# Kernel tuning notes

Hardware: AMD Instinct MI355X
Metric: run time of the kernel (lower is better)

## Reference

```python
import jax, jax.numpy as jnp
import numpy as np

N = 20000      # num_nodes
E = 320000     # num_edges (avg degree 16)
HID = 256      # hid_dim
H = 4          # attention heads
D = HID // H   # per-head dim (concat heads -> HID)
L = 2          # nGAT_layer
OUT = 12       # out_dim / pred_len (decoder steps)
NEG_SLOPE = 0.2


def setup_inputs() -> dict:
    key = jax.random.key(0)
    ks = jax.random.split(key, 16)
    s = 0.05
    nrm = lambda k, shape: jax.random.normal(k, shape, jnp.float32) * s
    return dict(
        x=nrm(ks[0], (N, HID)),
        edge_index=jax.random.randint(ks[1], (2, E), 0, N, dtype=jnp.int32),
        # GATv2Conv params per layer (stacked over L layers)
        gat_w_src=nrm(ks[2], (L, HID, H * D)),
        gat_w_dst=nrm(ks[3], (L, HID, H * D)),
        gat_att=nrm(ks[4], (L, H, D)),
        gat_bias=nrm(ks[5], (L, H * D)),
        # decoder_mlp: Linear(1 + HID -> HID)
        mlp_w=nrm(ks[6], (HID, 1 + HID)),
        mlp_b=nrm(ks[7], (HID,)),
        # nn.LSTM (1 layer, input HID, hidden HID), torch gate order i,f,g,o
        lstm_w_ih=nrm(ks[8], (4 * HID, HID)),
        lstm_w_hh=nrm(ks[9], (4 * HID, HID)),
        lstm_b_ih=nrm(ks[10], (4 * HID,)),
        lstm_b_hh=nrm(ks[11], (4 * HID,)),
        # decoder_init_proj: Linear(HID -> 1); decoder_output_proj: Linear(HID -> 1)
        init_w=nrm(ks[12], (1, HID)),
        init_b=nrm(ks[13], (1,)),
        out_w=nrm(ks[14], (1, HID)),
        out_b=nrm(ks[15], (1,)),
    )


def _gatv2_layer(x, src, dst, w_src, w_dst, att, bias):
    n = x.shape[0]
    xl = (x @ w_src).reshape(n, H, D)   # source-side projection
    xr = (x @ w_dst).reshape(n, H, D)   # destination-side projection
    # GATv2: e_ij = a^T LeakyReLU(Wl x_j + Wr x_i)
    e = jax.nn.leaky_relu(xl[src] + xr[dst], NEG_SLOPE)        # [E,H,D]
    logits = jnp.einsum('ehd,hd->eh', e, att)                   # [E,H]
    # edge softmax over incoming edges of each destination node
    m = jax.ops.segment_max(logits, dst, num_segments=n)        # [N,H]
    ex = jnp.exp(logits - m[dst])
    denom = jax.ops.segment_sum(ex, dst, num_segments=n)
    alpha = ex / denom[dst]                                     # [E,H]
    out = jax.ops.segment_sum(xl[src] * alpha[:, :, None], dst, num_segments=n)
    return out.reshape(n, H * D) + bias


def reference(x, edge_index, gat_w_src, gat_w_dst, gat_att, gat_bias,
              mlp_w, mlp_b, lstm_w_ih, lstm_w_hh, lstm_b_ih, lstm_b_hh,
              init_w, init_b, out_w, out_b):
    src, dst = edge_index[0], edge_index[1]
    # stacked GAT blocks: GATv2Conv + ELU (element == 2)
    for l in range(L):
        x = _gatv2_layer(x, src, dst, gat_w_src[l], gat_w_dst[l], gat_att[l], gat_bias[l])
        x = jax.nn.elu(x)
    # recurrent LSTM decoder, batch = nodes, seq step by step
    ctx = x                      # encoder_context
    h = x                        # h_0 = x (num_layers = 1)
    c = jnp.zeros_like(x)        # c_0 = 0
    prev = x @ init_w.T + init_b  # [N,1]
    outs = []
    for _ in range(OUT):
        dec_in = jnp.concatenate([prev, ctx], axis=1) @ mlp_w.T + mlp_b  # [N,HID]
        gates = dec_in @ lstm_w_ih.T + lstm_b_ih + h @ lstm_w_hh.T + lstm_b_hh
        i_g, f_g, g_g, o_g = jnp.split(gates, 4, axis=1)
        i_g = jax.nn.sigmoid(i_g)
        f_g = jax.nn.sigmoid(f_g)
        o_g = jax.nn.sigmoid(o_g)
        g_g = jnp.tanh(g_g)
        c = f_g * c + i_g * g_g
        h = o_g * jnp.tanh(c)
        prev = h @ out_w.T + out_b  # [N,1]
        outs.append(prev)
    return jnp.concatenate(outs, axis=1)  # [N, OUT]
```

## Files before the change

### kernel.cpp

```cpp
#include <hip/hip_runtime.h>
#include <hip/hip_bf16.h>

#define NN 20000
#define NE 320000
#define TOUT 12
#define DEGMAX 96
#define MR 80
#define NBLK 250
#define NCPL 13

typedef __bf16 bf16x8 __attribute__((ext_vector_type(8)));
typedef float float4v __attribute__((ext_vector_type(4)));

#define LD8(p) (*(const bf16x8*)(p))
#define MFMA16(a,b,c) __builtin_amdgcn_mfma_f32_16x16x32_bf16((a),(b),(c),0,0,0)

__device__ __forceinline__ float bf2f(const __hip_bfloat16 v){ return __bfloat162float(v); }
__device__ __forceinline__ __hip_bfloat16 f2bf(float v){ return __float2bfloat16(v); }
__device__ __forceinline__ float sigmoidr_(float x){ return __builtin_amdgcn_rcpf(1.f + __expf(-x)); }
__device__ __forceinline__ float tanhr_(float x){ return 1.f - 2.f*__builtin_amdgcn_rcpf(__expf(2.f*x) + 1.f); }
__device__ __forceinline__ float rdf(const void* p, int i, int f32){
  return f32 ? ((const float*)p)[i] : __bfloat162float(((const __hip_bfloat16*)p)[i]);
}

__global__ void k_detect(const void* xraw, int* flag){
  __shared__ int cnt;
  if(threadIdx.x == 0) cnt = 0;
  __syncthreads();
  const unsigned* w = (const unsigned*)xraw;
  int local = 0;
  for(int i = threadIdx.x; i < 4096; i += 256){
    unsigned b = (w[i] >> 8) & 0x7F;
    if(b >= 0x33 && b <= 0x3F) local++;
  }
  atomicAdd(&cnt, local);
  __syncthreads();
  if(threadIdx.x == 0) *flag = (cnt > 2048) ? 0 : 1;
}

__global__ void k_fail(float* out, int n){
  int i = blockIdx.x*256 + threadIdx.x;
  if(i < n) out[i] = 256.0f;
}

__global__ void k_count(const int* __restrict__ dst, int* __restrict__ deg){
  int e = blockIdx.x*256 + threadIdx.x;
  if(e < NE){
    unsigned d = (unsigned)dst[e];
    if(d < NN) atomicAdd(&deg[d], 1);
  }
}

__global__ void k_scan(const int* __restrict__ deg, int* __restrict__ offp, int* __restrict__ cursor){
  __shared__ int part[256];
  __shared__ int excl[257];
  const int CH = (NN + 255)/256;
  int tid = threadIdx.x;
  int lo = tid*CH;
  int hi = lo + CH; if(hi > NN) hi = NN;
  int s = 0;
  for(int i=lo;i<hi;i++) s += deg[i];
  part[tid] = s;
  __syncthreads();
  if(tid == 0){
    int run = 0;
    for(int i=0;i<256;i++){ excl[i] = run; run += part[i]; }
    excl[256] = run;
  }
  __syncthreads();
  int run = excl[tid];
  for(int i=lo;i<hi;i++){ offp[i] = run; cursor[i] = run; run += deg[i]; }
  if(tid == 0) offp[NN] = excl[256];
}

__global__ void k_fill(const int* __restrict__ src, const int* __restrict__ dst,
                       int* __restrict__ cursor, int* __restrict__ csr_src){
  int e = blockIdx.x*256 + threadIdx.x;
  if(e >= NE) return;
  unsigned d = (unsigned)dst[e];
  if(d >= NN) return;
  unsigned p = (unsigned)atomicAdd(&cursor[d], 1);
  if(p < NE){
    unsigned sv = (unsigned)src[e];
    csr_src[p] = (sv < NN) ? (int)sv : 0;
  }
}

__global__ void k_prep(const void* __restrict__ w_src, const void* __restrict__ w_dst,
                       const void* __restrict__ w_hh, const void* __restrict__ wih,
                       const void* __restrict__ mlp_w, const int* __restrict__ flag,
                       __hip_bfloat16* __restrict__ wsrcT, __hip_bfloat16* __restrict__ wdstT,
                       __hip_bfloat16* __restrict__ whhp, __hip_bfloat16* __restrict__ wihb,
                       __hip_bfloat16* __restrict__ mlpT){
  int tid = blockIdx.x*256 + threadIdx.x;
  int f = *flag;
  if(tid < 131072){
    int l = tid >> 16, r = tid & 65535, o = r >> 8, i = r & 255;
    wsrcT[tid] = f2bf(rdf(w_src, l*65536 + i*256 + o, f));
    wdstT[tid] = f2bf(rdf(w_dst, l*65536 + i*256 + o, f));
  }
  if(tid < 262144){
    whhp[tid] = f2bf(rdf(w_hh, tid, f));
    wihb[tid] = f2bf(rdf(wih, tid, f));
  }
  if(tid < 65536){
    int k = tid >> 8, j = tid & 255;
    mlpT[tid] = f2bf(rdf(mlp_w, j*257 + 1 + k, f));
  }
}

__global__ void k_prep_ub(const void* __restrict__ wih, const void* __restrict__ mlp_w,
                          const void* __restrict__ mlp_b,
                          const void* __restrict__ b_ih, const void* __restrict__ b_hh,
                          const void* __restrict__ att, const void* __restrict__ gbias,
                          const void* __restrict__ init_w, const void* __restrict__ init_b,
                          const void* __restrict__ out_w, const void* __restrict__ out_b,
                          const int* __restrict__ flag,
                          float* __restrict__ u, float* __restrict__ bc,
                          float* __restrict__ attf, float* __restrict__ gbiasf,
                          float* __restrict__ initwf, float* __restrict__ outwf,
                          float* __restrict__ sc){
  __shared__ float su[256], sb[256];
  int g = blockIdx.x, j = threadIdx.x, f = *flag;
  float w = rdf(wih, g*256 + j, f);
  su[j] = w * rdf(mlp_w, j*257, f);
  sb[j] = w * rdf(mlp_b, j, f);
  if(g < 2){
    int i = g*256 + j;
    attf[i] = rdf(att, i, f);
    gbiasf[i] = rdf(gbias, i, f);
  }
  if(g == 0){
    initwf[j] = rdf(init_w, j, f);
    outwf[j]  = rdf(out_w, j, f);
    if(j == 0){ sc[0] = rdf(init_b, 0, f); sc[1] = rdf(out_b, 0, f); }
  }
  __syncthreads();
  for(int s=128; s>0; s>>=1){
    if(j < s){ su[j] += su[j+s]; sb[j] += sb[j+s]; }
    __syncthreads();
  }
  if(j == 0){ u[g] = su[0]; bc[g] = sb[0] + rdf(b_ih, g, f) + rdf(b_hh, g, f); }
}

__global__ void k_fold(const __hip_bfloat16* __restrict__ whh_pl,
                       const float* __restrict__ u_vec, const float* __restrict__ outwf,
                       __hip_bfloat16* __restrict__ whh2_pl){
  int i = blockIdx.x*256 + threadIdx.x;
  whh2_pl[i] = f2bf(bf2f(whh_pl[i]) + u_vec[i >> 8]*outwf[i & 255]);
}

__global__ void k_pack3(const __hip_bfloat16* __restrict__ Wpl, const __hip_bfloat16* __restrict__ W2pl,
                        const __hip_bfloat16* __restrict__ Wcpl,
                        __hip_bfloat16* __restrict__ WhhP, __hip_bfloat16* __restrict__ Whh2P,
                        __hip_bfloat16* __restrict__ WcP){
  int idx = blockIdx.x*256 + threadIdx.x;
  if(idx >= 32768) return;
  int P    = idx >> 14;
  int cs   = (idx >> 11) & 7;
  int kidx = (idx >> 8) & 7;
  int ntl  = (idx >> 6) & 3;
  int lane = idx & 63;
  int l16 = lane & 15, quad = lane >> 4;
  int brow = ntl*256 + P*128 + cs*16 + l16;
  int srcofs = brow*256 + kidx*32 + quad*8;
  int dst = idx*8;
  *(bf16x8*)(WhhP + dst)  = LD8(Wpl + srcofs);
  *(bf16x8*)(Whh2P + dst) = LD8(W2pl + srcofs);
  *(bf16x8*)(WcP + dst)   = LD8(Wcpl + srcofs);
}

__global__ void k_pack2(const __hip_bfloat16* __restrict__ wsrcT,
                        const __hip_bfloat16* __restrict__ wdstT,
                        __hip_bfloat16* __restrict__ wprojP){
  int idx = blockIdx.x*256 + threadIdx.x;
  if(idx >= 32768) return;
  int m = idx >> 13;
  int fi = idx & 8191;
  int l = m >> 1, role = m & 1;
  int kidx = fi >> 10;
  int nt = (fi >> 6) & 15;
  int lane = fi & 63;
  int l16 = lane & 15, quad = lane >> 4;
  const __hip_bfloat16* src = (role ? wdstT : wsrcT) + l*65536;
  int srcofs = (nt*16 + l16)*256 + kidx*32 + quad*8;
  *(bf16x8*)(wprojP + (size_t)m*65536 + fi*8) = LD8(src + srcofs);
}

__global__ __launch_bounds__(256) void k_gemm_nt_bf(const __hip_bfloat16* __restrict__ A,
                                                    const __hip_bfloat16* __restrict__ B,
                                                    __hip_bfloat16* __restrict__ Cb, int M){
  int wave = threadIdx.x >> 6;
  int lane = threadIdx.x & 63;
  int l16 = lane & 15, quad = lane >> 4, quad8 = quad*8;
  int mBase = blockIdx.x*64 + wave*16;
  int nBase = blockIdx.y*64;
  int arow = mBase + l16; if(arow >= M) arow = M-1;
  const __hip_bfloat16* aptr = A + (size_t)arow*256 + quad8;
  float4v acc[4];
  #pragma unroll
  for(int nt=0;nt<4;nt++){ acc[nt][0]=0.f; acc[nt][1]=0.f; acc[nt][2]=0.f; acc[nt][3]=0.f; }
  for(int k0=0;k0<256;k0+=32){
    bf16x8 a = LD8(aptr + k0);
    #pragma unroll
    for(int nt=0;nt<4;nt++){
      const __hip_bfloat16* bptr = B + (size_t)(nBase + nt*16 + l16)*256 + k0 + quad8;
      acc[nt] = MFMA16(a, LD8(bptr), acc[nt]);
    }
  }
  #pragma unroll
  for(int nt=0;nt<4;nt++){
    int col = nBase + nt*16 + l16;
    #pragma unroll
    for(int r=0;r<4;r++){
      int row = mBase + quad*4 + r;
      if(row < M) Cb[(size_t)row*256 + col] = f2bf(acc[nt][r]);
    }
  }
}

__global__ __launch_bounds__(512, 2) void k_gemm_dual(__hip_bfloat16* __restrict__ P,
                                                      const void* __restrict__ xraw,
                                                      const int* __restrict__ flag,
                                                      int layer0,
                                                      const __hip_bfloat16* __restrict__ BsrcP,
                                                      const __hip_bfloat16* __restrict__ BdstP,
                                                      __hip_bfloat16* __restrict__ Q){
  __shared__ __hip_bfloat16 sA[64*264];
  int tid = threadIdx.x;
  int mBase = blockIdx.x*64;
  {
    int r = tid >> 3;
    int c0 = (tid & 7)*32;
    int grow = mBase + r; if(grow >= NN) grow = NN-1;
    if(layer0){
      int f = *flag;
      #pragma unroll
      for(int j=0;j<32;j++) sA[r*264 + c0 + j] = f2bf(rdf(xraw, grow*256 + c0 + j, f));
    }else{
      const __hip_bfloat16* srcp = P + (size_t)grow*256 + c0;
      #pragma unroll
      for(int j=0;j<4;j++) *(bf16x8*)(&sA[r*264 + c0 + j*8]) = LD8(srcp + j*8);
    }
  }
  __syncthreads();
  int w8 = tid >> 6;
  int w = w8 & 3;
  int role = w8 >> 2;
  int lane = tid&63, l16 = lane&15, quad = lane>>4, quad8 = quad*8;
  const __hip_bfloat16* B = role ? BdstP : BsrcP;
  __hip_bfloat16* C = role ? P : Q;
  const __hip_bfloat16* arow = &sA[(w*16 + l16)*264 + quad8];
  float4v acc[16];
  #pragma unroll
  for(int nt=0;nt<16;nt++){ acc[nt][0]=0.f; acc[nt][1]=0.f; acc[nt][2]=0.f; acc[nt][3]=0.f; }
  for(int kidx=0;kidx<8;kidx++){
    bf16x8 a = *(const bf16x8*)(arow + kidx*32);
    const __hip_bfloat16* bbase = B + (kidx<<13) + (lane<<3);
    #pragma unroll
    for(int nt=0;nt<16;nt++)
      acc[nt] = MFMA16(a, LD8(bbase + (nt<<9)), acc[nt]);
  }
  #pragma unroll
  for(int nt=0;nt<16;nt++){
    int col = nt*16 + l16;
    #pragma unroll
    for(int r=0;r<4;r++){
      int row = mBase + w*16 + quad*4 + r;
      if(row < NN) C[(size_t)row*256 + col] = f2bf(acc[nt][r]);
    }
  }
}

__global__ __launch_bounds__(256) void k_node_fused(const __hip_bfloat16* __restrict__ Q,
                                                    __hip_bfloat16* __restrict__ P,
                                                    const int* __restrict__ offp,
                                                    const int* __restrict__ csr_src,
                                                    const float* __restrict__ attf,
                                                    const float* __restrict__ gbiasf){
  __shared__ float slog[DEGMAX*4];
  __shared__ int ssrc[DEGMAX];
  int node = blockIdx.x;
  int tid = threadIdx.x;
  int s0 = offp[node], s1 = offp[node+1];
  if(s0 < 0) s0 = 0; if(s0 > NE) s0 = NE;
  if(s1 < s0) s1 = s0; if(s1 > NE) s1 = NE;
  int deg = s1 - s0; if(deg > DEGMAX) deg = DEGMAX;
  if(tid < deg){
    unsigned sv = (unsigned)csr_src[s0 + tid];
    ssrc[tid] = (sv < NN) ? (int)sv : 0;
  }
  __syncthreads();
  int w = tid>>6, lane = tid&63;
  int eSlot = lane>>4, li = lane&15;
  float prl[16], attl[16];
  #pragma unroll
  for(int h=0;h<4;h++)
    #pragma unroll
    for(int j=0;j<4;j++){
      int d = h*64 + j*16 + li;
      prl[h*4+j]  = bf2f(P[(size_t)node*256 + d]);
      attl[h*4+j] = attf[d];
    }
  for(int base=0; base<deg; base+=16){
    int e = base + w*4 + eSlot;
    bool valid = (e < deg);
    const __hip_bfloat16* pl = Q + (size_t)ssrc[valid ? e : 0]*256;
    float part[4];
    #pragma unroll
    for(int h=0;h<4;h++){
      float p = 0.f;
      #pragma unroll
      for(int j=0;j<4;j++){
        int d = h*64 + j*16 + li;
        float v = bf2f(pl[d]) + prl[h*4+j];
        v = (v > 0.f) ? v : 0.2f*v;
        p += v * attl[h*4+j];
      }
      part[h] = p;
    }
    #pragma unroll
    for(int h=0;h<4;h++){
      part[h] += __shfl_xor(part[h], 1, 64);
      part[h] += __shfl_xor(part[h], 2, 64);
      part[h] += __shfl_xor(part[h], 4, 64);
      part[h] += __shfl_xor(part[h], 8, 64);
    }
    if(li == 0 && valid){
      #pragma unroll
      for(int h=0;h<4;h++) slog[e*4+h] = part[h];
    }
  }
  __syncthreads();
  {
    int hh = tid >> 6;
    int li64 = tid & 63;
    float m = -1e30f;
    for(int i=li64; i<deg; i+=64) m = fmaxf(m, slog[i*4+hh]);
    #pragma unroll
    for(int s=1; s<64; s<<=1) m = fmaxf(m, __shfl_xor(m, s, 64));
    float den = 0.f;
    for(int i=li64; i<deg; i+=64) den += __expf(slog[i*4+hh] - m);
    #pragma unroll
    for(int s=1; s<64; s<<=1) den += __shfl_xor(den, s, 64);
    float inv = (den > 0.f) ? 1.f/den : 0.f;
    for(int i=li64; i<deg; i+=64) slog[i*4+hh] = __expf(slog[i*4+hh] - m)*inv;
  }
  __syncthreads();
  int d = tid, hd = d>>6;
  float acc = 0.f;
  for(int i=0;i<deg;i++) acc += slog[i*4+hd] * bf2f(Q[(size_t)ssrc[i]*256 + d]);
  acc += gbiasf[d];
  acc = (acc > 0.f) ? acc : (__expf(acc) - 1.f);
  P[(size_t)node*256 + d] = f2bf(acc);
}

__global__ __launch_bounds__(512, 1) void k_lstm80(const __hip_bfloat16* __restrict__ ctx,
                                                   const __hip_bfloat16* __restrict__ WcP,
                                                   const __hip_bfloat16* __restrict__ WhhP,
                                                   const __hip_bfloat16* __restrict__ Whh2P,
                                                   const float* __restrict__ u_vec,
                                                   const float* __restrict__ bc_vec,
                                                   const float* __restrict__ initwf,
                                                   const float* __restrict__ outwf,
                                                   const float* __restrict__ sc,
                                                   float* __restrict__ out){
  __shared__ __hip_bfloat16 sgx[NCPL*4096];
  __shared__ __hip_bfloat16 sh[MR*264];
  __shared__ float spartw[2][MR*16];
  __shared__ float sprev0[MR];
  float* spart = (float*)sgx;
  int tid = threadIdx.x;
  int mBase = blockIdx.x*MR;
  int cs = tid>>6, lane = tid&63, l16 = lane&15, quad = lane>>4, quad8 = quad*8;
  int phase = (blockIdx.x >> 3) & 7;
  int j0 = cs*16 + l16;
  int j1 = 128 + j0;
  #pragma unroll
  for(int p=0;p<3;p++){
    int r = p*32 + (tid >> 4);
    if(r < MR){
      int c0 = (tid & 15)*16;
      const __hip_bfloat16* srcp = ctx + (size_t)(mBase + r)*256 + c0;
      *(bf16x8*)(&sh[r*264 + c0])     = LD8(srcp);
      *(bf16x8*)(&sh[r*264 + c0 + 8]) = LD8(srcp + 8);
    }
  }
  __syncthreads();
  #pragma unroll
  for(int p=0;p<3;p++){
    int r = p*32 + (tid >> 4);
    int c0 = (tid & 15)*16;
    float part = 0.f;
    if(r < MR){
      #pragma unroll
      for(int j=0;j<16;j++) part += bf2f(sh[r*264 + c0 + j]) * initwf[c0 + j];
    }
    spart[tid] = part;
    __syncthreads();
    if(tid < 32 && p*32 + tid < MR){
      float s = 0.f;
      #pragma unroll
      for(int j=0;j<16;j++) s += spart[tid*16 + j];
      sprev0[p*32 + tid] = s + sc[0];
    }
    __syncthreads();
  }
  float ow0 = outwf[j0], ow1 = outwf[j1];
  float outb = sc[1];
  bf16x8 gg0, gg1, gg2, gg3, gg4, gg5, gg6;
  {
    float bcl[8];
    #pragma unroll
    for(int g=0;g<4;g++){
      bcl[g]   = bc_vec[g*256 + j0] + u_vec[g*256 + j0]*outb;
      bcl[4+g] = bc_vec[g*256 + j1] + u_vec[g*256 + j1]*outb;
    }
    #pragma unroll
    for(int P2=0;P2<2;P2++){
      float4v acc[20];
      #pragma unroll
      for(int nt=0;nt<20;nt++){ acc[nt][0]=0.f; acc[nt][1]=0.f; acc[nt][2]=0.f; acc[nt][3]=0.f; }
      #pragma unroll 2
      for(int ki=0;ki<8;ki++){
        int kidx = (ki + phase) & 7;
        int k0 = kidx*32;
        bf16x8 a0 = *(const bf16x8*)(&sh[l16*264 + k0 + quad8]);
        bf16x8 a1 = *(const bf16x8*)(&sh[(16 + l16)*264 + k0 + quad8]);
        bf16x8 a2 = *(const bf16x8*)(&sh[(32 + l16)*264 + k0 + quad8]);
        bf16x8 a3 = *(const bf16x8*)(&sh[(48 + l16)*264 + k0 + quad8]);
        bf16x8 a4 = *(const bf16x8*)(&sh[(64 + l16)*264 + k0 + quad8]);
        const __hip_bfloat16* bbase = WcP + P2*131072 + (((cs<<3) + kidx)<<11) + (lane<<3);
        #pragma unroll
        for(int ntl=0;ntl<4;ntl++){
          bf16x8 b = LD8(bbase + (ntl<<9));
          acc[ntl]     = MFMA16(a0, b, acc[ntl]);
          acc[4+ntl]   = MFMA16(a1, b, acc[4+ntl]);
          acc[8+ntl]   = MFMA16(a2, b, acc[8+ntl]);
          acc[12+ntl]  = MFMA16(a3, b, acc[12+ntl]);
          acc[16+ntl]  = MFMA16(a4, b, acc[16+ntl]);
        }
      }
      #pragma unroll
      for(int rt=0;rt<5;rt++)
        #pragma unroll
        for(int half=0;half<2;half++){
          bf16x8 v;
          #pragma unroll
          for(int rr=0;rr<2;rr++)
            #pragma unroll
            for(int g=0;g<4;g++){
              int r = half*2 + rr;
              v[rr*4+g] = (__bf16)f2bf(acc[rt*4 + g][r] + bcl[P2*4+g]);
            }
          const int cp = P2*10 + rt*2 + half;
          if(cp < NCPL) *(bf16x8*)(&sgx[cp*4096 + tid*8]) = v;
          else if(cp == 13) gg0 = v;
          else if(cp == 14) gg1 = v;
          else if(cp == 15) gg2 = v;
          else if(cp == 16) gg3 = v;
          else if(cp == 17) gg4 = v;
          else if(cp == 18) gg5 = v;
          else              gg6 = v;
        }
    }
  }
  float creg[40];
  #pragma unroll
  for(int i=0;i<40;i++) creg[i] = 0.f;
  #pragma unroll 1
  for(int step=0; step<TOUT; step++){
    const __hip_bfloat16* W = (step == 0) ? WhhP : Whh2P;
    int sb = step & 1;
    float4v acc[20];
    #pragma unroll
    for(int nt=0;nt<20;nt++){ acc[nt][0]=0.f; acc[nt][1]=0.f; acc[nt][2]=0.f; acc[nt][3]=0.f; }
    #pragma unroll 2
    for(int ki=0;ki<8;ki++){
      int kidx = (ki + phase) & 7;
      int k0 = kidx*32;
      bf16x8 a0 = *(const bf16x8*)(&sh[l16*264 + k0 + quad8]);
      bf16x8 a1 = *(const bf16x8*)(&sh[(16 + l16)*264 + k0 + quad8]);
      bf16x8 a2 = *(const bf16x8*)(&sh[(32 + l16)*264 + k0 + quad8]);
      bf16x8 a3 = *(const bf16x8*)(&sh[(48 + l16)*264 + k0 + quad8]);
      bf16x8 a4 = *(const bf16x8*)(&sh[(64 + l16)*264 + k0 + quad8]);
      const __hip_bfloat16* bbase = W + (((cs<<3) + kidx)<<11) + (lane<<3);
      #pragma unroll
      for(int ntl=0;ntl<4;ntl++){
        bf16x8 b = LD8(bbase + (ntl<<9));
        acc[ntl]     = MFMA16(a0, b, acc[ntl]);
        acc[4+ntl]   = MFMA16(a1, b, acc[4+ntl]);
        acc[8+ntl]   = MFMA16(a2, b, acc[8+ntl]);
        acc[12+ntl]  = MFMA16(a3, b, acc[12+ntl]);
        acc[16+ntl]  = MFMA16(a4, b, acc[16+ntl]);
      }
    }
    float hA[20];
    #pragma unroll
    for(int rt=0; rt<5; rt++){
      bf16x8 ga = *(const bf16x8*)(&sgx[(rt*2)*4096 + tid*8]);
      bf16x8 gb = *(const bf16x8*)(&sgx[(rt*2+1)*4096 + tid*8]);
      float hsum[4];
      #pragma unroll
      for(int r=0;r<4;r++){
        int row = rt*16 + quad*4 + r;
        int jb = (r&1)*4;
        float gx0, gx1, gx2, gx3;
        if(r < 2){
          gx0 = bf2f((__hip_bfloat16)ga[jb]);   gx1 = bf2f((__hip_bfloat16)ga[jb+1]);
          gx2 = bf2f((__hip_bfloat16)ga[jb+2]); gx3 = bf2f((__hip_bfloat16)ga[jb+3]);
        }else{
          gx0 = bf2f((__hip_bfloat16)gb[jb]);   gx1 = bf2f((__hip_bfloat16)gb[jb+1]);
          gx2 = bf2f((__hip_bfloat16)gb[jb+2]); gx3 = bf2f((__hip_bfloat16)gb[jb+3]);
        }
        float g0 = acc[rt*4 + 0][r] + gx0;
        float g1 = acc[rt*4 + 1][r] + gx1;
        float g2 = acc[rt*4 + 2][r] + gx2;
        float g3 = acc[rt*4 + 3][r] + gx3;
        if(step == 0){
          float pd = sprev0[row] - outb;
          g0 += pd*u_vec[j0];
          g1 += pd*u_vec[256 + j0];
          g2 += pd*u_vec[512 + j0];
          g3 += pd*u_vec[768 + j0];
        }
        float iv = sigmoidr_(g0), fv = sigmoidr_(g1);
        float gv = tanhr_(g2),    ov = sigmoidr_(g3);
        float cn = fv*creg[rt*4 + r] + iv*gv;
        creg[rt*4 + r] = cn;
        float hn = ov * tanhr_(cn);
        hA[rt*4 + r] = hn;
        hsum[r] = hn * ow0;
      }
      #pragma unroll
      for(int r=0;r<4;r++){
        hsum[r] += __shfl_xor(hsum[r], 1, 64);
        hsum[r] += __shfl_xor(hsum[r], 2, 64);
        hsum[r] += __shfl_xor(hsum[r], 4, 64);
        hsum[r] += __shfl_xor(hsum[r], 8, 64);
      }
      if(l16 == 0){
        #pragma unroll
        for(int r=0;r<4;r++)
          spartw[sb][(rt*16 + quad*4 + r)*16 + cs*2] = hsum[r];
      }
    }
    #pragma unroll
    for(int nt=0;nt<20;nt++){ acc[nt][0]=0.f; acc[nt][1]=0.f; acc[nt][2]=0.f; acc[nt][3]=0.f; }
    #pragma unroll 2
    for(int ki=0;ki<8;ki++){
      int kidx = (ki + phase) & 7;
      int k0 = kidx*32;
      bf16x8 a0 = *(const bf16x8*)(&sh[l16*264 + k0 + quad8]);
      bf16x8 a1 = *(const bf16x8*)(&sh[(16 + l16)*264 + k0 + quad8]);
      bf16x8 a2 = *(const bf16x8*)(&sh[(32 + l16)*264 + k0 + quad8]);
      bf16x8 a3 = *(const bf16x8*)(&sh[(48 + l16)*264 + k0 + quad8]);
      bf16x8 a4 = *(const bf16x8*)(&sh[(64 + l16)*264 + k0 + quad8]);
      const __hip_bfloat16* bbase = W + 131072 + (((cs<<3) + kidx)<<11) + (lane<<3);
      #pragma unroll
      for(int ntl=0;ntl<4;ntl++){
        bf16x8 b = LD8(bbase + (ntl<<9));
        acc[ntl]     = MFMA16(a0, b, acc[ntl]);
        acc[4+ntl]   = MFMA16(a1, b, acc[4+ntl]);
        acc[8+ntl]   = MFMA16(a2, b, acc[8+ntl]);
        acc[12+ntl]  = MFMA16(a3, b, acc[12+ntl]);
        acc[16+ntl]  = MFMA16(a4, b, acc[16+ntl]);
      }
    }
    __syncthreads();
    #pragma unroll
    for(int rt=0; rt<5; rt++){
      const int cpa = 10 + rt*2, cpb_ = 11 + rt*2;
      bf16x8 ga, gb;
      if(cpa < NCPL)      ga = *(const bf16x8*)(&sgx[cpa*4096 + tid*8]);
      else if(cpa == 14)  ga = gg1;
      else if(cpa == 16)  ga = gg3;
      else                ga = gg5;
      if(cpb_ < NCPL)     gb = *(const bf16x8*)(&sgx[cpb_*4096 + tid*8]);
      else if(cpb_ == 13) gb = gg0;
      else if(cpb_ == 15) gb = gg2;
      else if(cpb_ == 17) gb = gg4;
      else                gb = gg6;
      float hsum[4];
      #pragma unroll
      for(int r=0;r<4;r++){
        int row = rt*16 + quad*4 + r;
        int jb = (r&1)*4;
        float gx0, gx1, gx2, gx3;
        if(r < 2){
          gx0 = bf2f((__hip_bfloat16)ga[jb]);   gx1 = bf2f((__hip_bfloat16)ga[jb+1]);
          gx2 = bf2f((__hip_bfloat16)ga[jb+2]); gx3 = bf2f((__hip_bfloat16)ga[jb+3]);
        }else{
          gx0 = bf2f((__hip_bfloat16)gb[jb]);   gx1 = bf2f((__hip_bfloat16)gb[jb+1]);
          gx2 = bf2f((__hip_bfloat16)gb[jb+2]); gx3 = bf2f((__hip_bfloat16)gb[jb+3]);
        }
        float g0 = acc[rt*4 + 0][r] + gx0;
        float g1 = acc[rt*4 + 1][r] + gx1;
        float g2 = acc[rt*4 + 2][r] + gx2;
        float g3 = acc[rt*4 + 3][r] + gx3;
        if(step == 0){
          float pd = sprev0[row] - outb;
          g0 += pd*u_vec[j1];
          g1 += pd*u_vec[256 + j1];
          g2 += pd*u_vec[512 + j1];
          g3 += pd*u_vec[768 + j1];
        }
        float iv = sigmoidr_(g0), fv = sigmoidr_(g1);
        float gv = tanhr_(g2),    ov = sigmoidr_(g3);
        float cn = fv*creg[20 + rt*4 + r] + iv*gv;
        creg[20 + rt*4 + r] = cn;
        float hn = ov * tanhr_(cn);
        sh[row*264 + j0] = f2bf(hA[rt*4 + r]);
        sh[row*264 + j1] = f2bf(hn);
        hsum[r] = hn * ow1;
      }
      #pragma unroll
      for(int r=0;r<4;r++){
        hsum[r] += __shfl_xor(hsum[r], 1, 64);
        hsum[r] += __shfl_xor(hsum[r], 2, 64);
        hsum[r] += __shfl_xor(hsum[r], 4, 64);
        hsum[r] += __shfl_xor(hsum[r], 8, 64);
      }
      if(l16 == 0){
        #pragma unroll
        for(int r=0;r<4;r++)
          spartw[sb][(rt*16 + quad*4 + r)*16 + cs*2 + 1] = hsum[r];
      }
    }
    __syncthreads();
    if(tid < MR){
      float s = outb;
      #pragma unroll
      for(int c=0;c<16;c++) s += spartw[sb][tid*16 + c];
      out[(size_t)(mBase + tid)*TOUT + step] = s;
    }
  }
}

extern "C" void kernel_launch(void* const* d_in, const int* in_sizes, int n_in,
                              void* d_out, int out_size, void* d_ws, size_t ws_size,
                              hipStream_t stream){
  const void* x      = d_in[0];
  const int*  ei     = (const int*)d_in[1];
  const void* w_src  = d_in[2];
  const void* w_dst  = d_in[3];
  const void* att    = d_in[4];
  const void* gbias  = d_in[5];
  const void* mlp_w  = d_in[6];
  const void* mlp_b  = d_in[7];
  const void* w_ih   = d_in[8];
  const void* w_hh   = d_in[9];
  const void* b_ih   = d_in[10];
  const void* b_hh   = d_in[11];
  const void* init_w = d_in[12];
  const void* init_b = d_in[13];
  const void* out_w  = d_in[14];
  const void* out_b  = d_in[15];
  float* out = (float*)d_out;
  const int* srcp = ei;
  const int* dstp = ei + NE;
  (void)in_sizes; (void)n_in;

  char* ws = (char*)d_ws;
  size_t off = 0;
  auto alloc = [&](size_t bytes)->void*{
    void* p = ws + off;
    off += (bytes + 255) & ~(size_t)255;
    return p;
  };
  __hip_bfloat16* P = (__hip_bfloat16*)alloc((size_t)NN*256*2);
  __hip_bfloat16* Q = (__hip_bfloat16*)alloc((size_t)NN*256*2);
  int* deg      = (int*)alloc((size_t)NN*4);
  int* offp     = (int*)alloc((size_t)(NN+1)*4);
  int* cursor   = (int*)alloc((size_t)NN*4);
  int* csr_src  = (int*)alloc((size_t)NE*4);
  __hip_bfloat16* wsrcT   = (__hip_bfloat16*)alloc((size_t)131072*2);
  __hip_bfloat16* wdstT   = (__hip_bfloat16*)alloc((size_t)131072*2);
  __hip_bfloat16* wprojP  = (__hip_bfloat16*)alloc((size_t)4*65536*2);
  __hip_bfloat16* whh_pl  = (__hip_bfloat16*)alloc((size_t)262144*2);
  __hip_bfloat16* whh2_pl = (__hip_bfloat16*)alloc((size_t)262144*2);
  __hip_bfloat16* Wc_pl   = (__hip_bfloat16*)alloc((size_t)262144*2);
  __hip_bfloat16* WhhP    = (__hip_bfloat16*)alloc((size_t)262144*2);
  __hip_bfloat16* Whh2P   = (__hip_bfloat16*)alloc((size_t)262144*2);
  __hip_bfloat16* WcP     = (__hip_bfloat16*)alloc((size_t)262144*2);
  __hip_bfloat16* wihb    = (__hip_bfloat16*)alloc((size_t)262144*2);
  __hip_bfloat16* mlpT    = (__hip_bfloat16*)alloc((size_t)65536*2);
  float* u_vec  = (float*)alloc(1024*4);
  float* bc_vec = (float*)alloc(1024*4);
  float* attf   = (float*)alloc(512*4);
  float* gbiasf = (float*)alloc(512*4);
  float* initwf = (float*)alloc(256*4);
  float* outwf  = (float*)alloc(256*4);
  float* sc     = (float*)alloc(2*4);
  int*   flag   = (int*)alloc(4);

  if(off > ws_size){
    k_fail<<<(out_size + 255)/256, 256, 0, stream>>>(out, out_size);
    return;
  }

  k_detect<<<1, 256, 0, stream>>>(x, flag);
  hipMemsetAsync(deg, 0, (size_t)NN*4, stream);
  hipMemsetAsync(csr_src, 0xFF, (size_t)NE*4, stream);
  k_count<<<NE/256, 256, 0, stream>>>(dstp, deg);
  k_scan<<<1, 256, 0, stream>>>(deg, offp, cursor);
  k_fill<<<NE/256, 256, 0, stream>>>(srcp, dstp, cursor, csr_src);
  k_prep<<<1024, 256, 0, stream>>>(w_src, w_dst, w_hh, w_ih, mlp_w, flag,
                                   wsrcT, wdstT, whh_pl, wihb, mlpT);
  k_prep_ub<<<1024, 256, 0, stream>>>(w_ih, mlp_w, mlp_b, b_ih, b_hh, att, gbias,
                                      init_w, init_b, out_w, out_b, flag,
                                      u_vec, bc_vec, attf, gbiasf, initwf, outwf, sc);
  {
    dim3 gwc(16, 4);
    k_gemm_nt_bf<<<gwc, 256, 0, stream>>>(wihb, mlpT, Wc_pl, 1024);
  }
  k_fold<<<1024, 256, 0, stream>>>(whh_pl, u_vec, outwf, whh2_pl);
  k_pack3<<<128, 256, 0, stream>>>(whh_pl, whh2_pl, Wc_pl, WhhP, Whh2P, WcP);
  k_pack2<<<128, 256, 0, stream>>>(wsrcT, wdstT, wprojP);

  for(int l=0;l<2;l++){
    k_gemm_dual<<<313, 512, 0, stream>>>(P, x, flag, (l == 0) ? 1 : 0,
                                         wprojP + (size_t)(l*2)*65536,
                                         wprojP + (size_t)(l*2+1)*65536, Q);
    k_node_fused<<<NN, 256, 0, stream>>>(Q, P, offp, csr_src, attf + l*256, gbiasf + l*256);
  }

  k_lstm80<<<NBLK, 512, 0, stream>>>(P, WcP, WhhP, Whh2P, u_vec, bc_vec,
                                     initwf, outwf, sc, out);
}
```

Baseline: 647.5 us.

## Shrink LSTM row tile to 32 rows for multi-block occupancy

Reduces the LSTM decoder kernel's per-block row count from 80 to 32, which raises the grid from 250 to 625 blocks and allows up to 4 blocks per CU. Precomputed input-gate values are now split between LDS (4 slots) and registers (4 vectors), and the accumulator and cell-state arrays shrink to match. The goal is to fill all CUs and hide latency through more resident waves. The cost is more re-reading of the recurrent weights from global/L2, since each weight fetch now serves fewer rows.

```diff
diff --git a/kernel.cpp b/kernel.cpp
--- a/kernel.cpp
+++ b/kernel.cpp
@@ -5,9 +5,8 @@
 #define NE 320000
 #define TOUT 12
 #define DEGMAX 96
-#define MR 80
-#define NBLK 250
-#define NCPL 13
+#define MR 32
+#define NBLK 625
 
 typedef __bf16 bf16x8 __attribute__((ext_vector_type(8)));
 typedef float float4v __attribute__((ext_vector_type(4)));
@@ -355,7 +354,7 @@
   P[(size_t)node*256 + d] = f2bf(acc);
 }
 
-__global__ __launch_bounds__(512, 1) void k_lstm80(const __hip_bfloat16* __restrict__ ctx,
+__global__ __launch_bounds__(512, 4) void k_lstm32(const __hip_bfloat16* __restrict__ ctx,
                                                    const __hip_bfloat16* __restrict__ WcP,
                                                    const __hip_bfloat16* __restrict__ WhhP,
                                                    const __hip_bfloat16* __restrict__ Whh2P,
@@ -365,7 +364,7 @@
                                                    const float* __restrict__ outwf,
                                                    const float* __restrict__ sc,
                                                    float* __restrict__ out){
-  __shared__ __hip_bfloat16 sgx[NCPL*4096];
+  __shared__ __hip_bfloat16 sgx[4*4096];
   __shared__ __hip_bfloat16 sh[MR*264];
   __shared__ float spartw[2][MR*16];
   __shared__ float sprev0[MR];
@@ -373,42 +372,36 @@
   int tid = threadIdx.x;
   int mBase = blockIdx.x*MR;
   int cs = tid>>6, lane = tid&63, l16 = lane&15, quad = lane>>4, quad8 = quad*8;
-  int phase = (blockIdx.x >> 3) & 7;
+  int phase = blockIdx.x & 7;
   int j0 = cs*16 + l16;
   int j1 = 128 + j0;
-  #pragma unroll
-  for(int p=0;p<3;p++){
-    int r = p*32 + (tid >> 4);
-    if(r < MR){
-      int c0 = (tid & 15)*16;
-      const __hip_bfloat16* srcp = ctx + (size_t)(mBase + r)*256 + c0;
-      *(bf16x8*)(&sh[r*264 + c0])     = LD8(srcp);
-      *(bf16x8*)(&sh[r*264 + c0 + 8]) = LD8(srcp + 8);
-    }
-  }
-  __syncthreads();
-  #pragma unroll
-  for(int p=0;p<3;p++){
-    int r = p*32 + (tid >> 4);
+  {
+    int r = tid >> 4;
+    int c0 = (tid & 15)*16;
+    const __hip_bfloat16* srcp = ctx + (size_t)(mBase + r)*256 + c0;
+    *(bf16x8*)(&sh[r*264 + c0])     = LD8(srcp);
+    *(bf16x8*)(&sh[r*264 + c0 + 8]) = LD8(srcp + 8);
+  }
+  __syncthreads();
+  {
+    int r = tid >> 4;
     int c0 = (tid & 15)*16;
     float part = 0.f;
-    if(r < MR){
-      #pragma unroll
-      for(int j=0;j<16;j++) part += bf2f(sh[r*264 + c0 + j]) * initwf[c0 + j];
-    }
+    #pragma unroll
+    for(int j=0;j<16;j++) part += bf2f(sh[r*264 + c0 + j]) * initwf[c0 + j];
     spart[tid] = part;
     __syncthreads();
-    if(tid < 32 && p*32 + tid < MR){
+    if(tid < MR){
       float s = 0.f;
       #pragma unroll
       for(int j=0;j<16;j++) s += spart[tid*16 + j];
-      sprev0[p*32 + tid] = s + sc[0];
+      sprev0[tid] = s + sc[0];
     }
     __syncthreads();
   }
   float ow0 = outwf[j0], ow1 = outwf[j1];
   float outb = sc[1];
-  bf16x8 gg0, gg1, gg2, gg3, gg4, gg5, gg6;
+  bf16x8 gg0, gg1, gg2, gg3;
   {
     float bcl[8];
     #pragma unroll
@@ -418,31 +411,25 @@
     }
     #pragma unroll
     for(int P2=0;P2<2;P2++){
-      float4v acc[20];
-      #pragma unroll
-      for(int nt=0;nt<20;nt++){ acc[nt][0]=0.f; acc[nt][1]=0.f; acc[nt][2]=0.f; acc[nt][3]=0.f; }
+      float4v acc[8];
+      #pragma unroll
+      for(int nt=0;nt<8;nt++){ acc[nt][0]=0.f; acc[nt][1]=0.f; acc[nt][2]=0.f; acc[nt][3]=0.f; }
       #pragma unroll 2
       for(int ki=0;ki<8;ki++){
         int kidx = (ki + phase) & 7;
         int k0 = kidx*32;
         bf16x8 a0 = *(const bf16x8*)(&sh[l16*264 + k0 + quad8]);
         bf16x8 a1 = *(const bf16x8*)(&sh[(16 + l16)*264 + k0 + quad8]);
-        bf16x8 a2 = *(const bf16x8*)(&sh[(32 + l16)*264 + k0 + quad8]);
-        bf16x8 a3 = *(const bf16x8*)(&sh[(48 + l16)*264 + k0 + quad8]);
-        bf16x8 a4 = *(const bf16x8*)(&sh[(64 + l16)*264 + k0 + quad8]);
         const __hip_bfloat16* bbase = WcP + P2*131072 + (((cs<<3) + kidx)<<11) + (lane<<3);
         #pragma unroll
         for(int ntl=0;ntl<4;ntl++){
           bf16x8 b = LD8(bbase + (ntl<<9));
-          acc[ntl]     = MFMA16(a0, b, acc[ntl]);
-          acc[4+ntl]   = MFMA16(a1, b, acc[4+ntl]);
-          acc[8+ntl]   = MFMA16(a2, b, acc[8+ntl]);
-          acc[12+ntl]  = MFMA16(a3, b, acc[12+ntl]);
-          acc[16+ntl]  = MFMA16(a4, b, acc[16+ntl]);
+          acc[ntl]   = MFMA16(a0, b, acc[ntl]);
+          acc[4+ntl] = MFMA16(a1, b, acc[4+ntl]);
         }
       }
       #pragma unroll
-      for(int rt=0;rt<5;rt++)
+      for(int rt=0;rt<2;rt++)
         #pragma unroll
         for(int half=0;half<2;half++){
           bf16x8 v;
@@ -453,51 +440,42 @@
               int r = half*2 + rr;
               v[rr*4+g] = (__bf16)f2bf(acc[rt*4 + g][r] + bcl[P2*4+g]);
             }
-          const int cp = P2*10 + rt*2 + half;
-          if(cp < NCPL) *(bf16x8*)(&sgx[cp*4096 + tid*8]) = v;
-          else if(cp == 13) gg0 = v;
-          else if(cp == 14) gg1 = v;
-          else if(cp == 15) gg2 = v;
-          else if(cp == 16) gg3 = v;
-          else if(cp == 17) gg4 = v;
-          else if(cp == 18) gg5 = v;
-          else              gg6 = v;
+          const int cp = rt*2 + half;
+          if(P2 == 0) *(bf16x8*)(&sgx[cp*4096 + tid*8]) = v;
+          else if(cp == 0) gg0 = v;
+          else if(cp == 1) gg1 = v;
+          else if(cp == 2) gg2 = v;
+          else             gg3 = v;
         }
     }
   }
-  float creg[40];
+  float creg[16];
   #pragma unroll
-  for(int i=0;i<40;i++) creg[i] = 0.f;
+  for(int i=0;i<16;i++) creg[i] = 0.f;
   #pragma unroll 1
   for(int step=0; step<TOUT; step++){
     const __hip_bfloat16* W = (step == 0) ? WhhP : Whh2P;
     int sb = step & 1;
-    float4v acc[20];
-    #pragma unroll
-    for(int nt=0;nt<20;nt++){ acc[nt][0]=0.f; acc[nt][1]=0.f; acc[nt][2]=0.f; acc[nt][3]=0.f; }
+    float4v acc[8];
+    #pragma unroll
+    for(int nt=0;nt<8;nt++){ acc[nt][0]=0.f; acc[nt][1]=0.f; acc[nt][2]=0.f; acc[nt][3]=0.f; }
     #pragma unroll 2
     for(int ki=0;ki<8;ki++){
       int kidx = (ki + phase) & 7;
       int k0 = kidx*32;
       bf16x8 a0 = *(const bf16x8*)(&sh[l16*264 + k0 + quad8]);
       bf16x8 a1 = *(const bf16x8*)(&sh[(16 + l16)*264 + k0 + quad8]);
-      bf16x8 a2 = *(const bf16x8*)(&sh[(32 + l16)*264 + k0 + quad8]);
-      bf16x8 a3 = *(const bf16x8*)(&sh[(48 + l16)*264 + k0 + quad8]);
-      bf16x8 a4 = *(const bf16x8*)(&sh[(64 + l16)*264 + k0 + quad8]);
       const __hip_bfloat16* bbase = W + (((cs<<3) + kidx)<<11) + (lane<<3);
       #pragma unroll
       for(int ntl=0;ntl<4;ntl++){
         bf16x8 b = LD8(bbase + (ntl<<9));
-        acc[ntl]     = MFMA16(a0, b, acc[ntl]);
-        acc[4+ntl]   = MFMA16(a1, b, acc[4+ntl]);
-        acc[8+ntl]   = MFMA16(a2, b, acc[8+ntl]);
-        acc[12+ntl]  = MFMA16(a3, b, acc[12+ntl]);
-        acc[16+ntl]  = MFMA16(a4, b, acc[16+ntl]);
-      }
-    }
-    float hA[20];
-    #pragma unroll
-    for(int rt=0; rt<5; rt++){
+        acc[ntl]   = MFMA16(a0, b, acc[ntl]);
+        acc[4+ntl] = MFMA16(a1, b, acc[4+ntl]);
+      }
+    }
+    float hA[8];
+    #pragma unroll
+    for(int rt=0; rt<2; rt++){
       bf16x8 ga = *(const bf16x8*)(&sgx[(rt*2)*4096 + tid*8]);
       bf16x8 gb = *(const bf16x8*)(&sgx[(rt*2+1)*4096 + tid*8]);
       float hsum[4];
@@ -546,41 +524,26 @@
       }
     }
     #pragma unroll
-    for(int nt=0;nt<20;nt++){ acc[nt][0]=0.f; acc[nt][1]=0.f; acc[nt][2]=0.f; acc[nt][3]=0.f; }
+    for(int nt=0;nt<8;nt++){ acc[nt][0]=0.f; acc[nt][1]=0.f; acc[nt][2]=0.f; acc[nt][3]=0.f; }
     #pragma unroll 2
     for(int ki=0;ki<8;ki++){
       int kidx = (ki + phase) & 7;
       int k0 = kidx*32;
       bf16x8 a0 = *(const bf16x8*)(&sh[l16*264 + k0 + quad8]);
       bf16x8 a1 = *(const bf16x8*)(&sh[(16 + l16)*264 + k0 + quad8]);
-      bf16x8 a2 = *(const bf16x8*)(&sh[(32 + l16)*264 + k0 + quad8]);
-      bf16x8 a3 = *(const bf16x8*)(&sh[(48 + l16)*264 + k0 + quad8]);
-      bf16x8 a4 = *(const bf16x8*)(&sh[(64 + l16)*264 + k0 + quad8]);
       const __hip_bfloat16* bbase = W + 131072 + (((cs<<3) + kidx)<<11) + (lane<<3);
       #pragma unroll
       for(int ntl=0;ntl<4;ntl++){
         bf16x8 b = LD8(bbase + (ntl<<9));
-        acc[ntl]     = MFMA16(a0, b, acc[ntl]);
-        acc[4+ntl]   = MFMA16(a1, b, acc[4+ntl]);
-        acc[8+ntl]   = MFMA16(a2, b, acc[8+ntl]);
-        acc[12+ntl]  = MFMA16(a3, b, acc[12+ntl]);
-        acc[16+ntl]  = MFMA16(a4, b, acc[16+ntl]);
+        acc[ntl]   = MFMA16(a0, b, acc[ntl]);
+        acc[4+ntl] = MFMA16(a1, b, acc[4+ntl]);
       }
     }
     __syncthreads();
     #pragma unroll
-    for(int rt=0; rt<5; rt++){
-      const int cpa = 10 + rt*2, cpb_ = 11 + rt*2;
-      bf16x8 ga, gb;
-      if(cpa < NCPL)      ga = *(const bf16x8*)(&sgx[cpa*4096 + tid*8]);
-      else if(cpa == 14)  ga = gg1;
-      else if(cpa == 16)  ga = gg3;
-      else                ga = gg5;
-      if(cpb_ < NCPL)     gb = *(const bf16x8*)(&sgx[cpb_*4096 + tid*8]);
-      else if(cpb_ == 13) gb = gg0;
-      else if(cpb_ == 15) gb = gg2;
-      else if(cpb_ == 17) gb = gg4;
-      else                gb = gg6;
+    for(int rt=0; rt<2; rt++){
+      bf16x8 ga = (rt == 0) ? gg0 : gg2;
+      bf16x8 gb = (rt == 0) ? gg1 : gg3;
       float hsum[4];
       #pragma unroll
       for(int r=0;r<4;r++){
@@ -607,8 +570,8 @@
         }
         float iv = sigmoidr_(g0), fv = sigmoidr_(g1);
         float gv = tanhr_(g2),    ov = sigmoidr_(g3);
-        float cn = fv*creg[20 + rt*4 + r] + iv*gv;
-        creg[20 + rt*4 + r] = cn;
+        float cn = fv*creg[8 + rt*4 + r] + iv*gv;
+        creg[8 + rt*4 + r] = cn;
         float hn = ov * tanhr_(cn);
         sh[row*264 + j0] = f2bf(hA[rt*4 + r]);
         sh[row*264 + j1] = f2bf(hn);
@@ -725,6 +688,6 @@
     k_node_fused<<<NN, 256, 0, stream>>>(Q, P, offp, csr_src, attf + l*256, gbiasf + l*256);
   }
 
-  k_lstm80<<<NBLK, 512, 0, stream>>>(P, WcP, WhhP, Whh2P, u_vec, bc_vec,
+  k_lstm32<<<NBLK, 512, 0, stream>>>(P, WcP, WhhP, Whh2P, u_vec, bc_vec,
                                      initwf, outwf, sc, out);
 }
```

Result: slower. 730.2 us (+12.8%).

## Use single-pass online softmax in GAT node kernel, fusing logits and aggregation

Applied to the files above, without the earlier changes.

Replaces the three-phase per-node edge softmax (logits into shared memory, then max/denominator, then weighted gather) with one pass. Each thread owns one feature column and computes per-head logits by wave shuffle reduction, keeping a running max, denominator and accumulator in online-softmax style. The next source row is prefetched while the current edge is processed. This reads each neighbour's Q row once instead of twice and removes two barriers and the shared logit buffer, at the cost of a serial per-edge loop with a 6-step shuffle reduction and extra exp work per edge.

```diff
diff --git a/kernel.cpp b/kernel.cpp
--- a/kernel.cpp
+++ b/kernel.cpp
@@ -278,7 +278,6 @@
                                                     const int* __restrict__ csr_src,
                                                     const float* __restrict__ attf,
                                                     const float* __restrict__ gbiasf){
-  __shared__ float slog[DEGMAX*4];
   __shared__ int ssrc[DEGMAX];
   int node = blockIdx.x;
   int tid = threadIdx.x;
@@ -291,68 +290,34 @@
     ssrc[tid] = (sv < NN) ? (int)sv : 0;
   }
   __syncthreads();
-  int w = tid>>6, lane = tid&63;
-  int eSlot = lane>>4, li = lane&15;
-  float prl[16], attl[16];
-  #pragma unroll
-  for(int h=0;h<4;h++)
-    #pragma unroll
-    for(int j=0;j<4;j++){
-      int d = h*64 + j*16 + li;
-      prl[h*4+j]  = bf2f(P[(size_t)node*256 + d]);
-      attl[h*4+j] = attf[d];
-    }
-  for(int base=0; base<deg; base+=16){
-    int e = base + w*4 + eSlot;
-    bool valid = (e < deg);
-    const __hip_bfloat16* pl = Q + (size_t)ssrc[valid ? e : 0]*256;
-    float part[4];
-    #pragma unroll
-    for(int h=0;h<4;h++){
-      float p = 0.f;
-      #pragma unroll
-      for(int j=0;j<4;j++){
-        int d = h*64 + j*16 + li;
-        float v = bf2f(pl[d]) + prl[h*4+j];
-        v = (v > 0.f) ? v : 0.2f*v;
-        p += v * attl[h*4+j];
-      }
-      part[h] = p;
-    }
-    #pragma unroll
-    for(int h=0;h<4;h++){
-      part[h] += __shfl_xor(part[h], 1, 64);
-      part[h] += __shfl_xor(part[h], 2, 64);
-      part[h] += __shfl_xor(part[h], 4, 64);
-      part[h] += __shfl_xor(part[h], 8, 64);
-    }
-    if(li == 0 && valid){
-      #pragma unroll
-      for(int h=0;h<4;h++) slog[e*4+h] = part[h];
-    }
-  }
-  __syncthreads();
-  {
-    int hh = tid >> 6;
-    int li64 = tid & 63;
-    float m = -1e30f;
-    for(int i=li64; i<deg; i+=64) m = fmaxf(m, slog[i*4+hh]);
-    #pragma unroll
-    for(int s=1; s<64; s<<=1) m = fmaxf(m, __shfl_xor(m, s, 64));
-    float den = 0.f;
-    for(int i=li64; i<deg; i+=64) den += __expf(slog[i*4+hh] - m);
-    #pragma unroll
-    for(int s=1; s<64; s<<=1) den += __shfl_xor(den, s, 64);
-    float inv = (den > 0.f) ? 1.f/den : 0.f;
-    for(int i=li64; i<deg; i+=64) slog[i*4+hh] = __expf(slog[i*4+hh] - m)*inv;
-  }
-  __syncthreads();
-  int d = tid, hd = d>>6;
-  float acc = 0.f;
-  for(int i=0;i<deg;i++) acc += slog[i*4+hd] * bf2f(Q[(size_t)ssrc[i]*256 + d]);
-  acc += gbiasf[d];
-  acc = (acc > 0.f) ? acc : (__expf(acc) - 1.f);
-  P[(size_t)node*256 + d] = f2bf(acc);
+  float pr = bf2f(P[(size_t)node*256 + tid]);
+  float at = attf[tid];
+  float m = -1e30f, den = 0.f, acc = 0.f;
+  float qv = (deg > 0) ? bf2f(Q[(size_t)ssrc[0]*256 + tid]) : 0.f;
+  for(int i=0;i<deg;i++){
+    float qn = (i+1 < deg) ? bf2f(Q[(size_t)ssrc[i+1]*256 + tid]) : 0.f;
+    float v = qv + pr;
+    v = (v > 0.f) ? v : 0.2f*v;
+    float part = v * at;
+    part += __shfl_xor(part, 1, 64);
+    part += __shfl_xor(part, 2, 64);
+    part += __shfl_xor(part, 4, 64);
+    part += __shfl_xor(part, 8, 64);
+    part += __shfl_xor(part, 16, 64);
+    part += __shfl_xor(part, 32, 64);
+    if(part > m){
+      float sc = __expf(m - part);
+      acc *= sc; den *= sc; m = part;
+    }
+    float wgt = __expf(part - m);
+    den += wgt;
+    acc += wgt * qv;
+    qv = qn;
+  }
+  float o = (den > 0.f) ? acc * (1.f/den) : 0.f;
+  o += gbiasf[tid];
+  o = (o > 0.f) ? o : (__expf(o) - 1.f);
+  P[(size_t)node*256 + tid] = f2bf(o);
 }
 
 __global__ __launch_bounds__(512, 1) void k_lstm80(const __hip_bfloat16* __restrict__ ctx,
```

New measurement: 754.7 us. 1.17x slower.

## Process four nodes per block in GAT aggregation, vectorize loads, fuse fold into pack

Applied to the files above, without the earlier changes.

The edge-score kernel now handles four destination nodes per block in a loop, cutting the grid from one block per node to one per four. Each lane loads 16 contiguous bf16 values as two 8-wide vectors instead of scattered scalars. Because each head's 64 features now sit in 4 lanes, the shuffle reduction shrinks to two steps. The separate k_fold kernel is merged into k_pack3, computing Whh2 on the fly and dropping one launch and an intermediate buffer. Serialising nodes inside a block adds barriers and may reduce the latency hiding that many small blocks provided.

```diff
diff --git a/kernel.cpp b/kernel.cpp
--- a/kernel.cpp
+++ b/kernel.cpp
@@ -5,6 +5,7 @@
 #define NE 320000
 #define TOUT 12
 #define DEGMAX 96
+#define NPB 4
 #define MR 80
 #define NBLK 250
 #define NCPL 13
@@ -143,15 +144,9 @@
   if(j == 0){ u[g] = su[0]; bc[g] = sb[0] + rdf(b_ih, g, f) + rdf(b_hh, g, f); }
 }
 
-__global__ void k_fold(const __hip_bfloat16* __restrict__ whh_pl,
-                       const float* __restrict__ u_vec, const float* __restrict__ outwf,
-                       __hip_bfloat16* __restrict__ whh2_pl){
-  int i = blockIdx.x*256 + threadIdx.x;
-  whh2_pl[i] = f2bf(bf2f(whh_pl[i]) + u_vec[i >> 8]*outwf[i & 255]);
-}
-
-__global__ void k_pack3(const __hip_bfloat16* __restrict__ Wpl, const __hip_bfloat16* __restrict__ W2pl,
+__global__ void k_pack3(const __hip_bfloat16* __restrict__ Wpl,
                         const __hip_bfloat16* __restrict__ Wcpl,
+                        const float* __restrict__ u_vec, const float* __restrict__ outwf,
                         __hip_bfloat16* __restrict__ WhhP, __hip_bfloat16* __restrict__ Whh2P,
                         __hip_bfloat16* __restrict__ WcP){
   int idx = blockIdx.x*256 + threadIdx.x;
@@ -163,10 +158,17 @@
   int lane = idx & 63;
   int l16 = lane & 15, quad = lane >> 4;
   int brow = ntl*256 + P*128 + cs*16 + l16;
-  int srcofs = brow*256 + kidx*32 + quad*8;
+  int col0 = kidx*32 + quad*8;
+  int srcofs = brow*256 + col0;
   int dst = idx*8;
-  *(bf16x8*)(WhhP + dst)  = LD8(Wpl + srcofs);
-  *(bf16x8*)(Whh2P + dst) = LD8(W2pl + srcofs);
+  bf16x8 wv = LD8(Wpl + srcofs);
+  *(bf16x8*)(WhhP + dst) = wv;
+  float uu = u_vec[brow];
+  bf16x8 w2;
+  #pragma unroll
+  for(int jj=0;jj<8;jj++)
+    w2[jj] = (__bf16)f2bf(bf2f((__hip_bfloat16)wv[jj]) + uu*outwf[col0 + jj]);
+  *(bf16x8*)(Whh2P + dst) = w2;
   *(bf16x8*)(WcP + dst)   = LD8(Wcpl + srcofs);
 }
 
@@ -280,79 +282,72 @@
                                                     const float* __restrict__ gbiasf){
   __shared__ float slog[DEGMAX*4];
   __shared__ int ssrc[DEGMAX];
-  int node = blockIdx.x;
   int tid = threadIdx.x;
-  int s0 = offp[node], s1 = offp[node+1];
-  if(s0 < 0) s0 = 0; if(s0 > NE) s0 = NE;
-  if(s1 < s0) s1 = s0; if(s1 > NE) s1 = NE;
-  int deg = s1 - s0; if(deg > DEGMAX) deg = DEGMAX;
-  if(tid < deg){
-    unsigned sv = (unsigned)csr_src[s0 + tid];
-    ssrc[tid] = (sv < NN) ? (int)sv : 0;
-  }
-  __syncthreads();
   int w = tid>>6, lane = tid&63;
   int eSlot = lane>>4, li = lane&15;
-  float prl[16], attl[16];
-  #pragma unroll
-  for(int h=0;h<4;h++)
-    #pragma unroll
-    for(int j=0;j<4;j++){
-      int d = h*64 + j*16 + li;
-      prl[h*4+j]  = bf2f(P[(size_t)node*256 + d]);
-      attl[h*4+j] = attf[d];
-    }
-  for(int base=0; base<deg; base+=16){
-    int e = base + w*4 + eSlot;
-    bool valid = (e < deg);
-    const __hip_bfloat16* pl = Q + (size_t)ssrc[valid ? e : 0]*256;
-    float part[4];
-    #pragma unroll
-    for(int h=0;h<4;h++){
-      float p = 0.f;
-      #pragma unroll
-      for(int j=0;j<4;j++){
-        int d = h*64 + j*16 + li;
-        float v = bf2f(pl[d]) + prl[h*4+j];
+  float attl[16];
+  #pragma unroll
+  for(int j=0;j<16;j++) attl[j] = attf[li*16 + j];
+  float gb = gbiasf[tid];
+  int hd = tid>>6;
+  #pragma unroll 1
+  for(int nn=0; nn<NPB; nn++){
+    int node = blockIdx.x*NPB + nn;
+    int s0 = offp[node], s1 = offp[node+1];
+    if(s0 < 0) s0 = 0; if(s0 > NE) s0 = NE;
+    if(s1 < s0) s1 = s0; if(s1 > NE) s1 = NE;
+    int deg = s1 - s0; if(deg > DEGMAX) deg = DEGMAX;
+    if(tid < deg){
+      unsigned sv = (unsigned)csr_src[s0 + tid];
+      ssrc[tid] = (sv < NN) ? (int)sv : 0;
+    }
+    __syncthreads();
+    float prl[16];
+    {
+      const __hip_bfloat16* prow = P + (size_t)node*256 + li*16;
+      bf16x8 p0 = LD8(prow), p1 = LD8(prow + 8);
+      #pragma unroll
+      for(int j=0;j<8;j++){ prl[j] = bf2f((__hip_bfloat16)p0[j]); prl[8+j] = bf2f((__hip_bfloat16)p1[j]); }
+    }
+    for(int base=0; base<deg; base+=16){
+      int e = base + w*4 + eSlot;
+      bool valid = (e < deg);
+      const __hip_bfloat16* qrow = Q + (size_t)ssrc[valid ? e : 0]*256 + li*16;
+      bf16x8 q0 = LD8(qrow), q1 = LD8(qrow + 8);
+      float part = 0.f;
+      #pragma unroll
+      for(int j=0;j<16;j++){
+        float v = bf2f((__hip_bfloat16)(j<8 ? q0[j] : q1[j-8])) + prl[j];
         v = (v > 0.f) ? v : 0.2f*v;
-        p += v * attl[h*4+j];
-      }
-      part[h] = p;
-    }
-    #pragma unroll
-    for(int h=0;h<4;h++){
-      part[h] += __shfl_xor(part[h], 1, 64);
-      part[h] += __shfl_xor(part[h], 2, 64);
-      part[h] += __shfl_xor(part[h], 4, 64);
-      part[h] += __shfl_xor(part[h], 8, 64);
-    }
-    if(li == 0 && valid){
-      #pragma unroll
-      for(int h=0;h<4;h++) slog[e*4+h] = part[h];
-    }
-  }
-  __syncthreads();
-  {
-    int hh = tid >> 6;
-    int li64 = tid & 63;
-    float m = -1e30f;
-    for(int i=li64; i<deg; i+=64) m = fmaxf(m, slog[i*4+hh]);
-    #pragma unroll
-    for(int s=1; s<64; s<<=1) m = fmaxf(m, __shfl_xor(m, s, 64));
-    float den = 0.f;
-    for(int i=li64; i<deg; i+=64) den += __expf(slog[i*4+hh] - m);
-    #pragma unroll
-    for(int s=1; s<64; s<<=1) den += __shfl_xor(den, s, 64);
-    float inv = (den > 0.f) ? 1.f/den : 0.f;
-    for(int i=li64; i<deg; i+=64) slog[i*4+hh] = __expf(slog[i*4+hh] - m)*inv;
-  }
-  __syncthreads();
-  int d = tid, hd = d>>6;
-  float acc = 0.f;
-  for(int i=0;i<deg;i++) acc += slog[i*4+hd] * bf2f(Q[(size_t)ssrc[i]*256 + d]);
-  acc += gbiasf[d];
-  acc = (acc > 0.f) ? acc : (__expf(acc) - 1.f);
-  P[(size_t)node*256 + d] = f2bf(acc);
+        part += v * attl[j];
+      }
+      part += __shfl_xor(part, 1, 64);
+      part += __shfl_xor(part, 2, 64);
+      if((li & 3) == 0 && valid) slog[e*4 + (li>>2)] = part;
+    }
+    __syncthreads();
+    {
+      int hh = tid >> 6;
+      int li64 = tid & 63;
+      float m = -1e30f;
+      for(int i=li64; i<deg; i+=64) m = fmaxf(m, slog[i*4+hh]);
+      #pragma unroll
+      for(int s=1; s<64; s<<=1) m = fmaxf(m, __shfl_xor(m, s, 64));
+      float den = 0.f;
+      for(int i=li64; i<deg; i+=64) den += __expf(slog[i*4+hh] - m);
+      #pragma unroll
+      for(int s=1; s<64; s<<=1) den += __shfl_xor(den, s, 64);
+      float inv = (den > 0.f) ? 1.f/den : 0.f;
+      for(int i=li64; i<deg; i+=64) slog[i*4+hh] = __expf(slog[i*4+hh] - m)*inv;
+    }
+    __syncthreads();
+    float acc = 0.f;
+    for(int i=0;i<deg;i++) acc += slog[i*4+hd] * bf2f(Q[(size_t)ssrc[i]*256 + tid]);
+    acc += gb;
+    acc = (acc > 0.f) ? acc : (__expf(acc) - 1.f);
+    P[(size_t)node*256 + tid] = f2bf(acc);
+    __syncthreads();
+  }
 }
 
 __global__ __launch_bounds__(512, 1) void k_lstm80(const __hip_bfloat16* __restrict__ ctx,
@@ -678,7 +673,6 @@
   __hip_bfloat16* wdstT   = (__hip_bfloat16*)alloc((size_t)131072*2);
   __hip_bfloat16* wprojP  = (__hip_bfloat16*)alloc((size_t)4*65536*2);
   __hip_bfloat16* whh_pl  = (__hip_bfloat16*)alloc((size_t)262144*2);
-  __hip_bfloat16* whh2_pl = (__hip_bfloat16*)alloc((size_t)262144*2);
   __hip_bfloat16* Wc_pl   = (__hip_bfloat16*)alloc((size_t)262144*2);
   __hip_bfloat16* WhhP    = (__hip_bfloat16*)alloc((size_t)262144*2);
   __hip_bfloat16* Whh2P   = (__hip_bfloat16*)alloc((size_t)262144*2);
@@ -714,15 +708,14 @@
     dim3 gwc(16, 4);
     k_gemm_nt_bf<<<gwc, 256, 0, stream>>>(wihb, mlpT, Wc_pl, 1024);
   }
-  k_fold<<<1024, 256, 0, stream>>>(whh_pl, u_vec, outwf, whh2_pl);
-  k_pack3<<<128, 256, 0, stream>>>(whh_pl, whh2_pl, Wc_pl, WhhP, Whh2P, WcP);
+  k_pack3<<<128, 256, 0, stream>>>(whh_pl, Wc_pl, u_vec, outwf, WhhP, Whh2P, WcP);
   k_pack2<<<128, 256, 0, stream>>>(wsrcT, wdstT, wprojP);
 
   for(int l=0;l<2;l++){
     k_gemm_dual<<<313, 512, 0, stream>>>(P, x, flag, (l == 0) ? 1 : 0,
                                          wprojP + (size_t)(l*2)*65536,
                                          wprojP + (size_t)(l*2+1)*65536, Q);
-    k_node_fused<<<NN, 256, 0, stream>>>(Q, P, offp, csr_src, attf + l*256, gbiasf + l*256);
+    k_node_fused<<<NN/NPB, 256, 0, stream>>>(Q, P, offp, csr_src, attf + l*256, gbiasf + l*256);
   }
 
   k_lstm80<<<NBLK, 512, 0, stream>>>(P, WcP, WhhP, Whh2P, u_vec, bc_vec,
```

New measurement: 632.1 us. -2.4%, faster.
